# Performance work log

Measured on AMD Instinct MI355X. Metric: run time of the kernel, lower is better.

The kernel has to match this reference:

```python
import jax, jax.numpy as jnp
import numpy as np

D, DFF, H = 768, 3072, 12
HD = D // H
EPS = 1e-12

def _ln(t, gamma, beta):
    mu = t.mean(-1, keepdims=True)
    var = jnp.mean((t - mu) ** 2, -1, keepdims=True)
    return gamma * (t - mu) / jnp.sqrt(var + EPS) + beta

def setup_inputs() -> dict:
    key = jax.random.key(0)
    ks = jax.random.split(key, 16)
    s = 0.02
    x = jax.random.normal(ks[0], (2, 2048, D), jnp.float32)
    mask = jnp.ones((2, 2048), jnp.float32)
    def lin(k, out_d, in_d):
        kw, kb = jax.random.split(k)
        return (jax.random.normal(kw, (out_d, in_d), jnp.float32) * s,
                jnp.zeros((out_d,), jnp.float32))
    Wq, bq = lin(ks[1], D, D)
    Wk, bk = lin(ks[2], D, D)
    Wv, bv = lin(ks[3], D, D)
    Wp, bp = lin(ks[4], D, D)
    W1, bf1 = lin(ks[5], DFF, D)
    W2, bf2 = lin(ks[6], D, DFF)
    g1 = jnp.ones((D,), jnp.float32); be1 = jnp.zeros((D,), jnp.float32)
    g2 = jnp.ones((D,), jnp.float32); be2 = jnp.zeros((D,), jnp.float32)
    return dict(x=x, mask=mask, Wq=Wq, bq=bq, Wk=Wk, bk=bk, Wv=Wv, bv=bv,
                Wp=Wp, bp=bp, g1=g1, be1=be1, W1=W1, bf1=bf1, W2=W2, bf2=bf2,
                g2=g2, be2=be2)

def reference(x, mask, Wq, bq, Wk, bk, Wv, bv, Wp, bp, g1, be1, W1, bf1, W2, bf2, g2, be2):
    B, S, _ = x.shape
    # projections (torch Linear: x @ W^T + b)
    q = (x @ Wq.T + bq).reshape(B, S, H, HD).transpose(0, 2, 1, 3)  # [B,H,S,HD]
    k = (x @ Wk.T + bk).reshape(B, S, H, HD).transpose(0, 2, 1, 3)
    v = (x @ Wv.T + bv).reshape(B, S, H, HD).transpose(0, 2, 1, 3)
    scores = jnp.einsum('bhqd,bhkd->bhqk', q, k) / jnp.sqrt(jnp.float32(HD))
    scores = scores - 10000.0 * (1.0 - mask[:, None, None, :])
    p = jax.nn.softmax(scores, axis=-1)  # dropout is identity at eval
    h = jnp.einsum('bhqk,bhkd->bqhd', p, v).reshape(B, S, D)
    h = h @ Wp.T + bp
    x1 = _ln(x + h, g1, be1)
    ff = jax.nn.gelu(x1 @ W1.T + bf1, approximate=False) @ W2.T + bf2
    return _ln(x1 + ff, g2, be2)
```

## Files before the change

kernel.cpp:

```cpp
#include <hip/hip_runtime.h>
#include <hip/hip_bf16.h>
#include <math.h>

#define D_MODEL 768
#define D_FF    3072
#define N_HEAD  12
#define HEAD_D  64
#define BATCH   2
#define SEQ     2048
#define QKV_LD  2304

typedef __attribute__((ext_vector_type(8))) short short8;
typedef __attribute__((ext_vector_type(8))) unsigned short ushort8;
typedef __attribute__((ext_vector_type(4))) float f32x4;

__device__ inline unsigned short f2bf(float f) {
    union { __hip_bfloat16 b; unsigned short u; } cv;
    cv.b = __float2bfloat16(f);
    return cv.u;
}

__device__ inline float bf2f(unsigned short u) {
    union { unsigned int i; float f; } cv;
    cv.i = ((unsigned int)u) << 16;
    return cv.f;
}

__device__ inline void async_load16(const void* g, void* l) {
    __builtin_amdgcn_global_load_lds(
        (const __attribute__((address_space(1))) void*)g,
        (__attribute__((address_space(3))) void*)l, 16, 0, 0);
}

__global__ __launch_bounds__(256) void conv_fused(
    const float* __restrict__ x,
    const float* __restrict__ Wq, const float* __restrict__ Wk,
    const float* __restrict__ Wv, const float* __restrict__ Wp,
    const float* __restrict__ W1, const float* __restrict__ W2,
    const float* __restrict__ bq, const float* __restrict__ bk,
    const float* __restrict__ bv,
    unsigned short* __restrict__ xb, unsigned short* __restrict__ wqkvb,
    unsigned short* __restrict__ wpb, unsigned short* __restrict__ w1b,
    unsigned short* __restrict__ w2b, float* __restrict__ bqkv)
{
    int bid = blockIdx.x;
    const float* src; unsigned short* dst; int base;
    if      (bid < 3072) { src = x;  dst = xb;              base = bid;        }
    else if (bid < 3648) { src = Wq; dst = wqkvb;           base = bid - 3072; }
    else if (bid < 4224) { src = Wk; dst = wqkvb + 589824;  base = bid - 3648; }
    else if (bid < 4800) { src = Wv; dst = wqkvb + 1179648; base = bid - 4224; }
    else if (bid < 5376) { src = Wp; dst = wpb;             base = bid - 4800; }
    else if (bid < 7680) { src = W1; dst = w1b;             base = bid - 5376; }
    else if (bid < 9984) { src = W2; dst = w2b;             base = bid - 7680; }
    else {
        for (int j = threadIdx.x; j < QKV_LD; j += 256)
            bqkv[j] = (j < 768) ? bq[j] : (j < 1536) ? bk[j - 768] : bv[j - 1536];
        return;
    }
    int i = (base * 256 + threadIdx.x) * 4;
    float4 v = *(const float4*)(src + i);
    ushort4 o4;
    o4.x = f2bf(v.x); o4.y = f2bf(v.y); o4.z = f2bf(v.z); o4.w = f2bf(v.w);
    *(ushort4*)(dst + i) = o4;
}


template <int NS>
__global__ __launch_bounds__(256) void gemm_bf16(
    const unsigned short* __restrict__ A, int lda,
    const unsigned short* __restrict__ W, int ldw,
    const float* __restrict__ bias,
    const unsigned short* __restrict__ resb, int ldr,
    float* __restrict__ outf, unsigned short* __restrict__ outb,
    float* __restrict__ pacc, int ldo,
    int M, int N, int K, int mode)
{
    __shared__ unsigned short As[NS][128 * 32];
    __shared__ unsigned short Bs[NS][128 * 32];

    const int t    = threadIdx.x;
    const int lane = t & 63;
    const int wv   = t >> 6;
    const int wm   = wv >> 1;
    const int wn   = wv & 1;

    const int nxg  = gridDim.x;
    const int nwg  = nxg * gridDim.y;
    int flat = blockIdx.y * nxg + blockIdx.x;
    if ((nwg & 7) == 0) {
        const int cpx = nwg >> 3;
        flat = (flat & 7) * cpx + (flat >> 3);
    }
    const int bm   = (flat / nxg) * 128;
    const int bn   = (flat % nxg) * 128;

    const int kz   = blockIdx.z;
    const int Kc   = K / gridDim.z;

    const int qd   = lane >> 4;
    const int l16  = lane & 15;

    f32x4 acc[4][4];
    #pragma unroll
    for (int i = 0; i < 4; i++)
        #pragma unroll
        for (int j = 0; j < 4; j++)
            acc[i][j] = (f32x4){0.f, 0.f, 0.f, 0.f};

    const int srow = lane >> 2;
    const int sseg = (lane & 3) * 8;
    const int r0   = (wv * 2 + 0) * 16 + srow;
    const int r1   = (wv * 2 + 1) * 16 + srow;
    const size_t gA0 = (size_t)(bm + r0) * lda + sseg;
    const size_t gA1 = (size_t)(bm + r1) * lda + sseg;
    const size_t gB0 = (size_t)(bn + r0) * ldw + sseg;
    const size_t gB1 = (size_t)(bn + r1) * ldw + sseg;
    const int c0 = (wv * 2 + 0) * 512;
    const int c1 = (wv * 2 + 1) * 512;

    const int kbeg  = kz * Kc;
    const int niter = Kc / 32;

    async_load16(A + gA0 + kbeg, &As[0][c0]);
    async_load16(W + gB0 + kbeg, &Bs[0][c0]);
    async_load16(A + gA1 + kbeg, &As[0][c1]);
    async_load16(W + gB1 + kbeg, &Bs[0][c1]);
    if (niter > 1) {
        async_load16(A + gA0 + kbeg + 32, &As[1][c0]);
        async_load16(W + gB0 + kbeg + 32, &Bs[1][c0]);
        async_load16(A + gA1 + kbeg + 32, &As[1][c1]);
        async_load16(W + gB1 + kbeg + 32, &Bs[1][c1]);
    }
    if constexpr (NS == 4) {
        if (niter > 2) {
            async_load16(A + gA0 + kbeg + 64, &As[2][c0]);
            async_load16(W + gB0 + kbeg + 64, &Bs[2][c0]);
            async_load16(A + gA1 + kbeg + 64, &As[2][c1]);
            async_load16(W + gB1 + kbeg + 64, &Bs[2][c1]);
        }
    }

    int stage = 0;
    for (int it = 0; it < niter; it++) {
        if constexpr (NS == 4) {
            if      (it + 2 < niter) __builtin_amdgcn_s_waitcnt(0x0F78);
            else if (it + 1 < niter) __builtin_amdgcn_s_waitcnt(0x0F74);
            else                     __builtin_amdgcn_s_waitcnt(0x0F70);
        } else {
            if (it + 1 < niter) __builtin_amdgcn_s_waitcnt(0x0F74);
            else                __builtin_amdgcn_s_waitcnt(0x0F70);
        }
        __builtin_amdgcn_s_barrier();

        if (it + (NS - 1) < niter) {
            int sn = stage + (NS - 1);
            if (sn >= NS) sn -= NS;
            const int kn = kbeg + (it + (NS - 1)) * 32;
            async_load16(A + gA0 + kn, &As[sn][c0]);
            async_load16(W + gB0 + kn, &Bs[sn][c0]);
            async_load16(A + gA1 + kn, &As[sn][c1]);
            async_load16(W + gB1 + kn, &Bs[sn][c1]);
        }

        short8 af[4], bf[4];
        #pragma unroll
        for (int mt = 0; mt < 4; mt++)
            af[mt] = *(const short8*)(&As[stage][(wm * 64 + mt * 16 + l16) * 32 + qd * 8]);
        #pragma unroll
        for (int nt = 0; nt < 4; nt++)
            bf[nt] = *(const short8*)(&Bs[stage][(wn * 64 + nt * 16 + l16) * 32 + qd * 8]);
        #pragma unroll
        for (int mt = 0; mt < 4; mt++)
            #pragma unroll
            for (int nt = 0; nt < 4; nt++)
                acc[mt][nt] = __builtin_amdgcn_mfma_f32_16x16x32_bf16(
                    af[mt], bf[nt], acc[mt][nt], 0, 0, 0);

        stage = (stage == NS - 1) ? 0 : stage + 1;
    }

    #pragma unroll
    for (int mt = 0; mt < 4; mt++) {
        #pragma unroll
        for (int nt = 0; nt < 4; nt++) {
            int col = bn + wn * 64 + nt * 16 + l16;
            float bv = (kz == 0) ? bias[col] : 0.f;
            #pragma unroll
            for (int r = 0; r < 4; r++) {
                int row = bm + wm * 64 + mt * 16 + qd * 4 + r;
                if (kz != 0) {
                    pacc[(size_t)row * ldo + col] = acc[mt][nt][r];
                    continue;
                }
                float v = acc[mt][nt][r] + bv;
                if (mode == 1) {
                    v += bf2f(resb[(size_t)row * ldr + col]);
                    outf[(size_t)row * ldo + col] = v;
                } else if (mode == 2) {
                    v = 0.5f * v * (1.0f + erff(v * 0.70710678118654752f));
                    outb[(size_t)row * ldo + col] = f2bf(v);
                } else if (mode == 3) {
                    outb[(size_t)row * ldo + col] = f2bf(v);
                } else {
                    outf[(size_t)row * ldo + col] = v;
                }
            }
        }
    }
}

__global__ __launch_bounds__(256) void vtrans(
    const unsigned short* __restrict__ qkv, unsigned short* __restrict__ vT)
{
    __shared__ unsigned short T[64 * 72];
    const int t   = threadIdx.x;
    const int kt  = blockIdx.x;
    const int bh  = blockIdx.y;
    const int h   = bh % N_HEAD;
    const int b   = bh / N_HEAD;
    const int row = t >> 2;
    const int c0  = (t & 3) * 16;

    const unsigned short* src =
        qkv + (size_t)(b * SEQ + kt * 64 + row) * QKV_LD + 1536 + h * HEAD_D + c0;
    *(ushort8*)&T[row * 72 + c0]     = *(const ushort8*)src;
    *(ushort8*)&T[row * 72 + c0 + 8] = *(const ushort8*)(src + 8);
    __syncthreads();

    const int d = t >> 2;
    ushort8 o0, o1;
    #pragma unroll
    for (int j = 0; j < 8; j++) o0[j] = T[(c0 + j) * 72 + d];
    #pragma unroll
    for (int j = 0; j < 8; j++) o1[j] = T[(c0 + 8 + j) * 72 + d];
    unsigned short* dst = vT + ((size_t)bh * HEAD_D + d) * SEQ + kt * 64 + c0;
    *(ushort8*)dst       = o0;
    *(ushort8*)(dst + 8) = o1;
}

#define ASTR 72

__global__ __launch_bounds__(256) void attn_mfma(
    const unsigned short* __restrict__ qkv, const unsigned short* __restrict__ vT,
    const float* __restrict__ mask, unsigned short* __restrict__ out)
{
    __shared__ __align__(16) unsigned short Ks[64 * ASTR];
    __shared__ __align__(16) unsigned short Vt[64 * ASTR];
    __shared__ float Ms[64];

    const int t    = threadIdx.x;
    const int lane = t & 63;
    const int wv   = t >> 6;
    const int l16  = lane & 15;
    const int quad = lane >> 4;
    const int q0   = blockIdx.x * 64;
    const int bh   = blockIdx.y;
    const int h    = bh % N_HEAD;
    const int b    = bh / N_HEAD;

    const unsigned short* qb  = qkv + (size_t)b * SEQ * QKV_LD + h * HEAD_D;
    const unsigned short* kb  = qb + 768;
    const unsigned short* vtb = vT + (size_t)bh * HEAD_D * SEQ;

    const int srow = t >> 2;
    const int sc0  = (t & 3) * 16;
    const int sigrow = (srow & 0x23) | ((srow & 0x04) << 2) | ((srow & 0x18) >> 1);

    {
        const ushort8* src = (const ushort8*)(qb + (size_t)(q0 + srow) * QKV_LD + sc0);
        *(ushort8*)&Ks[srow * ASTR + sc0]     = src[0];
        *(ushort8*)&Ks[srow * ASTR + sc0 + 8] = src[1];
    }
    __syncthreads();
    short8 bq0 = *(const short8*)&Ks[(wv * 16 + l16) * ASTR + quad * 8];
    short8 bq1 = *(const short8*)&Ks[(wv * 16 + l16) * ASTR + 32 + quad * 8];
    __syncthreads();

    f32x4 o[4];
    #pragma unroll
    for (int i = 0; i < 4; i++) o[i] = (f32x4){0.f, 0.f, 0.f, 0.f};
    float m_st = -INFINITY, l_st = 0.f;

    ushort8 rk0, rk1, rv0, rv1;
    float rm = 1.0f;
    {
        const ushort8* ksrc = (const ushort8*)(kb + (size_t)srow * QKV_LD + sc0);
        rk0 = ksrc[0]; rk1 = ksrc[1];
        const ushort8* vsrc = (const ushort8*)(vtb + (size_t)srow * SEQ + sc0);
        rv0 = vsrc[0]; rv1 = vsrc[1];
        if (t < 64) rm = mask[b * SEQ + t];
    }

    for (int kt = 0; kt < SEQ / 64; kt++) {
        *(ushort8*)&Ks[sigrow * ASTR + sc0]     = rk0;
        *(ushort8*)&Ks[sigrow * ASTR + sc0 + 8] = rk1;
        *(ushort8*)&Vt[srow * ASTR + sc0]       = rv0;
        *(ushort8*)&Vt[srow * ASTR + sc0 + 8]   = rv1;
        if (t < 64) Ms[t] = -10000.0f * (1.0f - rm);
        __syncthreads();

        if (kt + 1 < SEQ / 64) {
            const int kn = (kt + 1) * 64;
            const ushort8* ksrc = (const ushort8*)(kb + (size_t)(kn + srow) * QKV_LD + sc0);
            rk0 = ksrc[0]; rk1 = ksrc[1];
            const ushort8* vsrc = (const ushort8*)(vtb + (size_t)srow * SEQ + kn + sc0);
            rv0 = vsrc[0]; rv1 = vsrc[1];
            if (t < 64) rm = mask[b * SEQ + kn + t];
        }

        f32x4 st[4];
        #pragma unroll
        for (int bi = 0; bi < 4; bi++) {
            const int krow = (bi * 16 + l16) * ASTR;
            short8 k0 = *(const short8*)&Ks[krow + quad * 8];
            short8 k1 = *(const short8*)&Ks[krow + 32 + quad * 8];
            f32x4 z = (f32x4){0.f, 0.f, 0.f, 0.f};
            z = __builtin_amdgcn_mfma_f32_16x16x32_bf16(k0, bq0, z, 0, 0, 0);
            st[bi] = __builtin_amdgcn_mfma_f32_16x16x32_bf16(k1, bq1, z, 0, 0, 0);
        }

        float p[4][4];
        float mx = -3.0e38f;
        #pragma unroll
        for (int bi = 0; bi < 4; bi++) {
            #pragma unroll
            for (int r = 0; r < 4; r++) {
                float s = fmaf(st[bi][r], 0.125f,
                               Ms[((bi >> 1) << 5) + (quad << 3) + ((bi & 1) << 2) + r]);
                p[bi][r] = s;
                mx = fmaxf(mx, s);
            }
        }
        mx = fmaxf(mx, __shfl_xor(mx, 16, 64));
        mx = fmaxf(mx, __shfl_xor(mx, 32, 64));
        float m_new = fmaxf(m_st, mx);
        float alpha = __expf(m_st - m_new);
        m_st = m_new;
        float ls = 0.f;
        #pragma unroll
        for (int bi = 0; bi < 4; bi++) {
            #pragma unroll
            for (int r = 0; r < 4; r++) {
                p[bi][r] = __expf(p[bi][r] - m_new);
                ls += p[bi][r];
            }
        }
        ls += __shfl_xor(ls, 16, 64);
        ls += __shfl_xor(ls, 32, 64);
        l_st = l_st * alpha + ls;

        float ar[4];
        #pragma unroll
        for (int r = 0; r < 4; r++) ar[r] = __shfl(alpha, quad * 4 + r, 64);
        #pragma unroll
        for (int nt = 0; nt < 4; nt++)
            #pragma unroll
            for (int r = 0; r < 4; r++)
                o[nt][r] *= ar[r];

        short8 pf0, pf1;
        #pragma unroll
        for (int bsel = 0; bsel < 2; bsel++) {
            #pragma unroll
            for (int r = 0; r < 4; r++) {
                pf0[bsel * 4 + r] = (short)f2bf(p[bsel][r]);
                pf1[bsel * 4 + r] = (short)f2bf(p[2 + bsel][r]);
            }
        }

        #pragma unroll
        for (int nt = 0; nt < 4; nt++) {
            const int vrow = (nt * 16 + l16) * ASTR;
            short8 v0 = *(const short8*)&Vt[vrow + quad * 8];
            short8 v1 = *(const short8*)&Vt[vrow + 32 + quad * 8];
            o[nt] = __builtin_amdgcn_mfma_f32_16x16x32_bf16(pf0, v0, o[nt], 0, 0, 0);
            o[nt] = __builtin_amdgcn_mfma_f32_16x16x32_bf16(pf1, v1, o[nt], 0, 0, 0);
        }
        __syncthreads();
    }

    float inv = 1.0f / l_st;
    float ir[4];
    #pragma unroll
    for (int r = 0; r < 4; r++) ir[r] = __shfl(inv, quad * 4 + r, 64);
    #pragma unroll
    for (int nt = 0; nt < 4; nt++) {
        #pragma unroll
        for (int r = 0; r < 4; r++) {
            int qi = q0 + wv * 16 + quad * 4 + r;
            out[(size_t)(b * SEQ + qi) * D_MODEL + h * HEAD_D + nt * 16 + l16] =
                f2bf(o[nt][r] * ir[r]);
        }
    }
}

__global__ __launch_bounds__(256) void ln_kernel(
    const float* __restrict__ in, const float* __restrict__ in2,
    const float* __restrict__ g, const float* __restrict__ be,
    float* __restrict__ outf, unsigned short* __restrict__ outb)
{
    const int row = blockIdx.x;
    const int t   = threadIdx.x;
    const float* rp  = in  + (size_t)row * D_MODEL;
    const float* rp2 = in2 ? in2 + (size_t)row * D_MODEL : nullptr;

    float vals[3];
    float s = 0.f, s2 = 0.f;
    #pragma unroll
    for (int i = 0; i < 3; i++) {
        float x = rp[t + i * 256];
        if (rp2) x += rp2[t + i * 256];
        vals[i] = x;
        s += x; s2 += x * x;
    }
    #pragma unroll
    for (int off = 32; off >= 1; off >>= 1) {
        s  += __shfl_xor(s,  off, 64);
        s2 += __shfl_xor(s2, off, 64);
    }
    __shared__ float rs[4], rs2[4];
    __shared__ float mu_s, rstd_s;
    const int wave = t >> 6, lane = t & 63;
    if (lane == 0) { rs[wave] = s; rs2[wave] = s2; }
    __syncthreads();
    if (t == 0) {
        float S1 = rs[0] + rs[1] + rs[2] + rs[3];
        float S2 = rs2[0] + rs2[1] + rs2[2] + rs2[3];
        float mu  = S1 * (1.0f / D_MODEL);
        float var = S2 * (1.0f / D_MODEL) - mu * mu;
        mu_s = mu;
        rstd_s = rsqrtf(var + 1e-12f);
    }
    __syncthreads();
    const float mu = mu_s, rstd = rstd_s;
    #pragma unroll
    for (int i = 0; i < 3; i++) {
        int c = t + i * 256;
        float o = g[c] * (vals[i] - mu) * rstd + be[c];
        if (outf) outf[(size_t)row * D_MODEL + c] = o;
        if (outb) outb[(size_t)row * D_MODEL + c] = f2bf(o);
    }
}

extern "C" void kernel_launch(void* const* d_in, const int* in_sizes, int n_in,
                              void* d_out, int out_size, void* d_ws, size_t ws_size,
                              hipStream_t stream)
{
    const float* x    = (const float*)d_in[0];
    const float* mask = (const float*)d_in[1];
    const float* Wq   = (const float*)d_in[2];
    const float* bq   = (const float*)d_in[3];
    const float* Wk   = (const float*)d_in[4];
    const float* bk   = (const float*)d_in[5];
    const float* Wv   = (const float*)d_in[6];
    const float* bv   = (const float*)d_in[7];
    const float* Wp   = (const float*)d_in[8];
    const float* bp   = (const float*)d_in[9];
    const float* g1   = (const float*)d_in[10];
    const float* be1  = (const float*)d_in[11];
    const float* W1   = (const float*)d_in[12];
    const float* bf1  = (const float*)d_in[13];
    const float* W2   = (const float*)d_in[14];
    const float* bf2  = (const float*)d_in[15];
    const float* g2   = (const float*)d_in[16];
    const float* be2  = (const float*)d_in[17];

    const int M = BATCH * SEQ;

    char* ws = (char*)d_ws;
    unsigned short* qkvb  = (unsigned short*)(ws + 0);
    unsigned short* ff1b  = (unsigned short*)(ws + 0);
    unsigned short* xb    = (unsigned short*)(ws + 25165824);
    unsigned short* hb    = (unsigned short*)(ws + 31457280);
    unsigned short* x1b   = (unsigned short*)(ws + 31457280);
    float*          y0    = (float*)(ws + 37748736);
    unsigned short* wqkvb = (unsigned short*)(ws + 50331648);
    unsigned short* wpb   = (unsigned short*)(ws + 53870592);
    unsigned short* w1b   = (unsigned short*)(ws + 55050240);
    unsigned short* w2b   = (unsigned short*)(ws + 59768832);
    float*          bqkv  = (float*)(ws + 64487424);
    float*          p1    = (float*)(ws + 64496640);
    unsigned short* vTb   = (unsigned short*)(ws + 77079552);

    dim3 blk(256);

    conv_fused<<<dim3(9985), blk, 0, stream>>>(
        x, Wq, Wk, Wv, Wp, W1, W2, bq, bk, bv,
        xb, wqkvb, wpb, w1b, w2b, bqkv);

    gemm_bf16<4><<<dim3(QKV_LD / 128, M / 128, 1), blk, 0, stream>>>(
        xb, D_MODEL, wqkvb, D_MODEL, bqkv, nullptr, 0,
        nullptr, qkvb, nullptr, QKV_LD, M, QKV_LD, D_MODEL, 3);

    vtrans<<<dim3(SEQ / 64, BATCH * N_HEAD), blk, 0, stream>>>(qkvb, vTb);

    attn_mfma<<<dim3(SEQ / 64, BATCH * N_HEAD), blk, 0, stream>>>(qkvb, vTb, mask, hb);

    gemm_bf16<4><<<dim3(D_MODEL / 128, M / 128, 2), blk, 0, stream>>>(
        hb, D_MODEL, wpb, D_MODEL, bp, xb, D_MODEL,
        y0, nullptr, p1, D_MODEL, M, D_MODEL, D_MODEL, 1);

    ln_kernel<<<dim3(M), blk, 0, stream>>>(y0, p1, g1, be1, nullptr, x1b);

    gemm_bf16<3><<<dim3(D_FF / 128, M / 128, 1), blk, 0, stream>>>(
        x1b, D_MODEL, w1b, D_MODEL, bf1, nullptr, 0,
        nullptr, ff1b, nullptr, D_FF, M, D_FF, D_MODEL, 2);

    gemm_bf16<4><<<dim3(D_MODEL / 128, M / 128, 2), blk, 0, stream>>>(
        ff1b, D_FF, w2b, D_FF, bf2, x1b, D_MODEL,
        y0, nullptr, p1, D_MODEL, M, D_MODEL, D_FF, 1);

    ln_kernel<<<dim3(M), blk, 0, stream>>>(y0, p1, g2, be2, (float*)d_out, nullptr);
}
```

Measured before the change: 381.1 us.

## Split attention along keys with merge kernel, add XCD-aware GEMM tile remap

The attention kernel now splits the key sequence in two along a new grid z dimension. Each half writes unnormalized fp32 partial outputs plus running max and sum, and a new merge kernel combines them into the bf16 head output. This doubles the attention grid to improve occupancy across CUs. In exchange it adds a launch and fp32 partial traffic. Separately, the GEMM tile swizzle becomes an XCD-aware grouped mapping with a per-launch group width. The projection and FFN2 GEMMs drop to 3 pipeline stages, and MFMA sections are bracketed with s_setprio.

```diff
diff --git a/kernel.cpp b/kernel.cpp
--- a/kernel.cpp
+++ b/kernel.cpp
@@ -73,7 +73,7 @@
     const unsigned short* __restrict__ resb, int ldr,
     float* __restrict__ outf, unsigned short* __restrict__ outb,
     float* __restrict__ pacc, int ldo,
-    int M, int N, int K, int mode)
+    int M, int N, int K, int mode, int rn)
 {
     __shared__ unsigned short As[NS][128 * 32];
     __shared__ unsigned short Bs[NS][128 * 32];
@@ -84,15 +84,17 @@
     const int wm   = wv >> 1;
     const int wn   = wv & 1;
 
-    const int nxg  = gridDim.x;
-    const int nwg  = nxg * gridDim.y;
-    int flat = blockIdx.y * nxg + blockIdx.x;
-    if ((nwg & 7) == 0) {
-        const int cpx = nwg >> 3;
-        flat = (flat & 7) * cpx + (flat >> 3);
-    }
-    const int bm   = (flat / nxg) * 128;
-    const int bn   = (flat % nxg) * 128;
+    const int nxg = gridDim.x;
+    const int cpx = (nxg * gridDim.y) >> 3;
+    const int flat = blockIdx.y * nxg + blockIdx.x;
+    const int xcd = flat & 7;
+    const int u   = flat >> 3;
+    const int rm  = cpx / rn;
+    const int rpr = nxg / rn;
+    const int mi  = (xcd / rpr) * rm + u / rn;
+    const int ni  = (xcd % rpr) * rn + u % rn;
+    const int bm  = mi * 128;
+    const int bn  = ni * 128;
 
     const int kz   = blockIdx.z;
     const int Kc   = K / gridDim.z;
@@ -242,7 +244,8 @@
 
 __global__ __launch_bounds__(256) void attn_mfma(
     const unsigned short* __restrict__ qkv, const unsigned short* __restrict__ vT,
-    const float* __restrict__ mask, unsigned short* __restrict__ out)
+    const float* __restrict__ mask,
+    float* __restrict__ o0p, float* __restrict__ o1p, float* __restrict__ mlbuf)
 {
     __shared__ __align__(16) unsigned short Ks[64 * ASTR];
     __shared__ __align__(16) unsigned short Vt[64 * ASTR];
@@ -255,8 +258,11 @@
     const int quad = lane >> 4;
     const int q0   = blockIdx.x * 64;
     const int bh   = blockIdx.y;
+    const int z    = blockIdx.z;
     const int h    = bh % N_HEAD;
     const int b    = bh / N_HEAD;
+    const int kt0  = z * (SEQ / 128);
+    const int ktE  = kt0 + (SEQ / 128);
 
     const unsigned short* qb  = qkv + (size_t)b * SEQ * QKV_LD + h * HEAD_D;
     const unsigned short* kb  = qb + 768;
@@ -284,14 +290,14 @@
     ushort8 rk0, rk1, rv0, rv1;
     float rm = 1.0f;
     {
-        const ushort8* ksrc = (const ushort8*)(kb + (size_t)srow * QKV_LD + sc0);
+        const ushort8* ksrc = (const ushort8*)(kb + (size_t)(kt0 * 64 + srow) * QKV_LD + sc0);
         rk0 = ksrc[0]; rk1 = ksrc[1];
-        const ushort8* vsrc = (const ushort8*)(vtb + (size_t)srow * SEQ + sc0);
+        const ushort8* vsrc = (const ushort8*)(vtb + (size_t)srow * SEQ + kt0 * 64 + sc0);
         rv0 = vsrc[0]; rv1 = vsrc[1];
-        if (t < 64) rm = mask[b * SEQ + t];
-    }
-
-    for (int kt = 0; kt < SEQ / 64; kt++) {
+        if (t < 64) rm = mask[b * SEQ + kt0 * 64 + t];
+    }
+
+    for (int kt = kt0; kt < ktE; kt++) {
         *(ushort8*)&Ks[sigrow * ASTR + sc0]     = rk0;
         *(ushort8*)&Ks[sigrow * ASTR + sc0 + 8] = rk1;
         *(ushort8*)&Vt[srow * ASTR + sc0]       = rv0;
@@ -299,7 +305,7 @@
         if (t < 64) Ms[t] = -10000.0f * (1.0f - rm);
         __syncthreads();
 
-        if (kt + 1 < SEQ / 64) {
+        if (kt + 1 < ktE) {
             const int kn = (kt + 1) * 64;
             const ushort8* ksrc = (const ushort8*)(kb + (size_t)(kn + srow) * QKV_LD + sc0);
             rk0 = ksrc[0]; rk1 = ksrc[1];
@@ -309,15 +315,17 @@
         }
 
         f32x4 st[4];
+        __builtin_amdgcn_s_setprio(1);
         #pragma unroll
         for (int bi = 0; bi < 4; bi++) {
             const int krow = (bi * 16 + l16) * ASTR;
             short8 k0 = *(const short8*)&Ks[krow + quad * 8];
             short8 k1 = *(const short8*)&Ks[krow + 32 + quad * 8];
-            f32x4 z = (f32x4){0.f, 0.f, 0.f, 0.f};
-            z = __builtin_amdgcn_mfma_f32_16x16x32_bf16(k0, bq0, z, 0, 0, 0);
-            st[bi] = __builtin_amdgcn_mfma_f32_16x16x32_bf16(k1, bq1, z, 0, 0, 0);
-        }
+            f32x4 zf = (f32x4){0.f, 0.f, 0.f, 0.f};
+            zf = __builtin_amdgcn_mfma_f32_16x16x32_bf16(k0, bq0, zf, 0, 0, 0);
+            st[bi] = __builtin_amdgcn_mfma_f32_16x16x32_bf16(k1, bq1, st[bi] = zf, 0, 0, 0);
+        }
+        __builtin_amdgcn_s_setprio(0);
 
         float p[4][4];
         float mx = -3.0e38f;
@@ -368,6 +376,7 @@
             }
         }
 
+        __builtin_amdgcn_s_setprio(1);
         #pragma unroll
         for (int nt = 0; nt < 4; nt++) {
             const int vrow = (nt * 16 + l16) * ASTR;
@@ -376,22 +385,52 @@
             o[nt] = __builtin_amdgcn_mfma_f32_16x16x32_bf16(pf0, v0, o[nt], 0, 0, 0);
             o[nt] = __builtin_amdgcn_mfma_f32_16x16x32_bf16(pf1, v1, o[nt], 0, 0, 0);
         }
+        __builtin_amdgcn_s_setprio(0);
         __syncthreads();
     }
 
-    float inv = 1.0f / l_st;
-    float ir[4];
-    #pragma unroll
-    for (int r = 0; r < 4; r++) ir[r] = __shfl(inv, quad * 4 + r, 64);
+    float* opart = (z == 0) ? o0p : o1p;
     #pragma unroll
     for (int nt = 0; nt < 4; nt++) {
         #pragma unroll
         for (int r = 0; r < 4; r++) {
             int qi = q0 + wv * 16 + quad * 4 + r;
-            out[(size_t)(b * SEQ + qi) * D_MODEL + h * HEAD_D + nt * 16 + l16] =
-                f2bf(o[nt][r] * ir[r]);
-        }
-    }
+            opart[((size_t)bh * SEQ + qi) * HEAD_D + nt * 16 + l16] = o[nt][r];
+        }
+    }
+    if (lane < 16) {
+        int q = q0 + wv * 16 + lane;
+        mlbuf[(z * 24 + bh) * SEQ + q]         = m_st;
+        mlbuf[98304 + (z * 24 + bh) * SEQ + q] = l_st;
+    }
+}
+
+__global__ __launch_bounds__(256) void attn_merge(
+    const float* __restrict__ o0p, const float* __restrict__ o1p,
+    const float* __restrict__ mlbuf, unsigned short* __restrict__ out)
+{
+    const int idx = blockIdx.x * 256 + threadIdx.x;
+    const int row = idx >> 4;
+    const int dq  = (idx & 15) * 4;
+    const int bh  = row >> 11, q = row & 2047;
+    const int b   = bh / N_HEAD, h = bh % N_HEAD;
+
+    const float m0 = mlbuf[row];
+    const float m1 = mlbuf[49152 + row];
+    const float l0 = mlbuf[98304 + row];
+    const float l1 = mlbuf[98304 + 49152 + row];
+    const float mx = fmaxf(m0, m1);
+    const float w0 = __expf(m0 - mx), w1 = __expf(m1 - mx);
+    const float inv = 1.0f / (l0 * w0 + l1 * w1);
+
+    const float4 a = *(const float4*)(o0p + (size_t)row * HEAD_D + dq);
+    const float4 c = *(const float4*)(o1p + (size_t)row * HEAD_D + dq);
+    ushort4 r4;
+    r4.x = f2bf((a.x * w0 + c.x * w1) * inv);
+    r4.y = f2bf((a.y * w0 + c.y * w1) * inv);
+    r4.z = f2bf((a.z * w0 + c.z * w1) * inv);
+    r4.w = f2bf((a.w * w0 + c.w * w1) * inv);
+    *(ushort4*)(out + ((size_t)(b * SEQ + q)) * D_MODEL + h * HEAD_D + dq) = r4;
 }
 
 __global__ __launch_bounds__(256) void ln_kernel(
@@ -481,6 +520,7 @@
     float*          bqkv  = (float*)(ws + 64487424);
     float*          p1    = (float*)(ws + 64496640);
     unsigned short* vTb   = (unsigned short*)(ws + 77079552);
+    float*          mlbuf = (float*)(ws + 50331648);
 
     dim3 blk(256);
 
@@ -490,25 +530,28 @@
 
     gemm_bf16<4><<<dim3(QKV_LD / 128, M / 128, 1), blk, 0, stream>>>(
         xb, D_MODEL, wqkvb, D_MODEL, bqkv, nullptr, 0,
-        nullptr, qkvb, nullptr, QKV_LD, M, QKV_LD, D_MODEL, 3);
+        nullptr, qkvb, nullptr, QKV_LD, M, QKV_LD, D_MODEL, 3, 9);
 
     vtrans<<<dim3(SEQ / 64, BATCH * N_HEAD), blk, 0, stream>>>(qkvb, vTb);
 
-    attn_mfma<<<dim3(SEQ / 64, BATCH * N_HEAD), blk, 0, stream>>>(qkvb, vTb, mask, hb);
-
-    gemm_bf16<4><<<dim3(D_MODEL / 128, M / 128, 2), blk, 0, stream>>>(
+    attn_mfma<<<dim3(SEQ / 64, BATCH * N_HEAD, 2), blk, 0, stream>>>(
+        qkvb, vTb, mask, y0, p1, mlbuf);
+
+    attn_merge<<<dim3(6144), blk, 0, stream>>>(y0, p1, mlbuf, hb);
+
+    gemm_bf16<3><<<dim3(D_MODEL / 128, M / 128, 2), blk, 0, stream>>>(
         hb, D_MODEL, wpb, D_MODEL, bp, xb, D_MODEL,
-        y0, nullptr, p1, D_MODEL, M, D_MODEL, D_MODEL, 1);
+        y0, nullptr, p1, D_MODEL, M, D_MODEL, D_MODEL, 1, 3);
 
     ln_kernel<<<dim3(M), blk, 0, stream>>>(y0, p1, g1, be1, nullptr, x1b);
 
     gemm_bf16<3><<<dim3(D_FF / 128, M / 128, 1), blk, 0, stream>>>(
         x1b, D_MODEL, w1b, D_MODEL, bf1, nullptr, 0,
-        nullptr, ff1b, nullptr, D_FF, M, D_FF, D_MODEL, 2);
-
-    gemm_bf16<4><<<dim3(D_MODEL / 128, M / 128, 2), blk, 0, stream>>>(
+        nullptr, ff1b, nullptr, D_FF, M, D_FF, D_MODEL, 2, 12);
+
+    gemm_bf16<3><<<dim3(D_MODEL / 128, M / 128, 2), blk, 0, stream>>>(
         ff1b, D_FF, w2b, D_FF, bf2, x1b, D_MODEL,
-        y0, nullptr, p1, D_MODEL, M, D_MODEL, D_FF, 1);
+        y0, nullptr, p1, D_MODEL, M, D_MODEL, D_FF, 1, 3);
 
     ln_kernel<<<dim3(M), blk, 0, stream>>>(y0, p1, g2, be2, (float*)d_out, nullptr);
 }
```

Result: slower. 395.9 us (+3.9%).
